# Kernel tuning notes

Measured on AMD Instinct MI355X. Metric: run time of the kernel, lower is better.

The kernel has to match this reference:

```python
import jax, jax.numpy as jnp
import numpy as np

M, NQ, NKV, DX, DT = 8, 1024, 1024, 512, 2
H, HD = 8, 64            # num_heads, head_dim
INNER = H * HD           # 512
KHID = 16                # kernel MLP hidden dim
SCALE = HD ** -0.5


def setup_inputs() -> dict:
    key = jax.random.key(0)
    ks = jax.random.split(key, 16)
    s = lambda fan_in: 1.0 / np.sqrt(fan_in)
    return {
        "xq": jax.random.normal(ks[0], (M, NQ, DX), jnp.float32),
        "xk": jax.random.normal(ks[1], (M, NKV, DX), jnp.float32),
        "xv": jax.random.normal(ks[2], (M, NKV, DX), jnp.float32),
        "tq": jax.random.normal(ks[3], (M, NQ, DT), jnp.float32),
        "tk": jax.random.normal(ks[4], (M, NKV, DT), jnp.float32),
        # attention projections (bias=False for q/k/v, Linear bias for out)
        "w_q": jax.random.normal(ks[5], (DX, INNER), jnp.float32) * s(DX),
        "w_k": jax.random.normal(ks[6], (DX, INNER), jnp.float32) * s(DX),
        "w_v": jax.random.normal(ks[7], (DX, INNER), jnp.float32) * s(DX),
        "w_out": jax.random.normal(ks[8], (INNER, DX), jnp.float32) * s(INNER),
        "b_out": jnp.zeros((DX,), jnp.float32),
        # kernel MLP: dt -> KHID -> H (per-head pairwise bias)
        "kw1": jax.random.normal(ks[9], (DT, KHID), jnp.float32) * s(DT),
        "kb1": jnp.zeros((KHID,), jnp.float32),
        "kw2": jax.random.normal(ks[10], (KHID, H), jnp.float32) * s(KHID),
        "kb2": jnp.zeros((H,), jnp.float32),
    }


def reference(xq, xk, xv, tq, tk, w_q, w_k, w_v, w_out, b_out, kw1, kb1, kw2, kb2):
    # pairwise differences of input locations: [m, nq, nkv, dt]
    diff = tq[:, :, None, :] - tk[:, None, :, :]
    # kernel MLP -> per-head bias, rearranged to [m, h, nq, nkv]
    hmid = jax.nn.relu(diff @ kw1 + kb1)          # [m, nq, nkv, KHID]
    dots = jnp.einsum('mqkc,ch->mhqk', hmid, kw2) + kb2[None, :, None, None]
    # token attention: standard scaled QK scores
    q = (xq @ w_q).reshape(M, NQ, H, HD)          # [m, nq, h, d]
    k = (xk @ w_k).reshape(M, NKV, H, HD)
    token_dots = jnp.einsum('mqhd,mkhd->mhqk', q, k) * SCALE
    dots = dots + token_dots
    attn = jax.nn.softmax(dots, axis=-1)          # softmax over keys
    v = (xv @ w_v).reshape(M, NKV, H, HD)
    out = jnp.einsum('mhqk,mkhd->mqhd', attn, v).reshape(M, NQ, INNER)
    return out @ w_out + b_out                    # [m, nq, dx]
```

## Files before the change

### kernel.cpp

```cpp
#include <hip/hip_runtime.h>


typedef unsigned short u16;
typedef unsigned int   u32;
typedef short bf8 __attribute__((ext_vector_type(8)));
typedef float f4  __attribute__((ext_vector_type(4)));
typedef _Float16 h2 __attribute__((ext_vector_type(2)));

#define Mb 8
#define SCALE 0.125f
#define NTOK 4194304

__device__ __forceinline__ u16 f2bf(float f) {
    union { float f; u32 u; } v; v.f = f;
    u32 r = v.u + 0x7fffu + ((v.u >> 16) & 1u);
    return (u16)(r >> 16);
}
__device__ __forceinline__ u32 pk2(float a, float b) {
    u32 r;
    asm("v_cvt_pk_bf16_f32 %0, %1, %2" : "=v"(r) : "v"(a), "v"(b));
    return r;
}
__device__ __forceinline__ void gl_lds16(const u16* g, u16* l) {
    __builtin_amdgcn_global_load_lds(
        (const __attribute__((address_space(1))) u32*)g,
        (__attribute__((address_space(3))) u32*)l, 16, 0, 0);
}
__device__ __forceinline__ h2 h2_of(u32 x) {
    union { u32 u; h2 h; } c; c.u = x; return c.h;
}
__device__ __forceinline__ u32 u_of(h2 x) {
    union { h2 h; u32 u; } c; c.h = x; return c.u;
}
__device__ __forceinline__ float dot2(h2 a, h2 b, float c) {
#if __has_builtin(__builtin_amdgcn_fdot2)
    return __builtin_amdgcn_fdot2(a, b, c, false);
#else
    return fmaf((float)a[0], (float)b[0], fmaf((float)a[1], (float)b[1], c));
#endif
}

struct PArgs {
    const float* ws[4];
    u16* dstW;
};

__global__ __launch_bounds__(256) void prep(PArgs p) {
    __shared__ u16 tl[64][80];
    const int tid = threadIdx.x;
    const int b = blockIdx.x;
    const int mat = b >> 6, t = b & 63;
    const int kt = t >> 3, nt = t & 7;
    const float* src = p.ws[mat] + (size_t)kt * 64 * 512 + (size_t)nt * 64;
    const int r0 = tid >> 4, c4 = (tid & 15) * 4;
    #pragma unroll
    for (int rr = 0; rr < 4; ++rr) {
        const int row = r0 + rr * 16;
        float4 a = *(const float4*)(src + (size_t)row * 512 + c4);
        tl[c4 + 0][row] = f2bf(a.x);
        tl[c4 + 1][row] = f2bf(a.y);
        tl[c4 + 2][row] = f2bf(a.z);
        tl[c4 + 3][row] = f2bf(a.w);
    }
    __syncthreads();
    u16* dst = p.dstW + (size_t)mat * 262144 + (size_t)nt * 64 * 512 + (size_t)kt * 64;
    #pragma unroll
    for (int i = 0; i < 2; ++i) {
        const int s2 = tid + i * 256;
        const int nrow = s2 >> 3, k8 = (s2 & 7) * 8;
        *(uint4*)(dst + (size_t)nrow * 512 + k8) = *(const uint4*)&tl[nrow][k8];
    }
}

struct GArgs {
    const void*  A[3];
    const u16*   W[3];
    void*        C[3];
    const float* bias;
    int          modeT[3];
    int          outf32;
    int          af32;
};

__global__ __launch_bounds__(256) void gemm_mfma(GArgs g) {
    __shared__ u16 Xs[128][32];
    __shared__ u16 Ws[128][32];

    const int z   = blockIdx.z;
    const int tid = threadIdx.x;
    const int w = tid >> 6, lane = tid & 63, quad = lane >> 4, l16 = lane & 15;
    const int wm = w >> 1, wn = w & 1;
    const int n0 = blockIdx.x * 128, t0 = blockIdx.y * 128;
    const int trans = g.modeT[z];

    f4 acc[4][4];
    #pragma unroll
    for (int i = 0; i < 4; ++i)
        #pragma unroll
        for (int j = 0; j < 4; ++j) acc[i][j] = (f4)0.f;

    const int lrow  = lane >> 2;
    const int kslot = (lane & 3) ^ ((lane >> 3) & 3);
    u16* ldsW0 = &Ws[w * 32][0];
    u16* ldsW1 = &Ws[w * 32 + 16][0];
    const u16* gW0 = g.W[z] + (size_t)(n0 + w * 32 + lrow) * 512 + kslot * 8;
    const u16* gW1 = gW0 + 16 * 512;

    u16* ldsX0 = &Xs[w * 32][0];
    u16* ldsX1 = &Xs[w * 32 + 16][0];
    const u16* gA0 = (const u16*)g.A[z] + (size_t)(t0 + w * 32 + lrow) * 512 + kslot * 8;
    const u16* gA1 = gA0 + 16 * 512;

    const int arow_s = tid >> 1, ah = tid & 1;
    const float* aF = (const float*)g.A[z] + (size_t)(t0 + arow_s) * 512 + ah * 16;
    const int s_sw = (arow_s >> 1) & 3;
    u16* aw0 = &Xs[arow_s][((2 * ah)     ^ s_sw) * 8];
    u16* aw1 = &Xs[arow_s][((2 * ah + 1) ^ s_sw) * 8];

    const int rslot = (quad ^ ((l16 >> 1) & 3)) * 8;

    float4 f0, f1, f2, f3;
    if (g.af32) {
        f0 = *(const float4*)(aF + 0);
        f1 = *(const float4*)(aF + 4);
        f2 = *(const float4*)(aF + 8);
        f3 = *(const float4*)(aF + 12);
    }

    for (int kc = 0; kc < 512; kc += 32) {
        __syncthreads();
        if (g.af32) {
            uint4 v0, v1;
            v0.x = pk2(f0.x, f0.y); v0.y = pk2(f0.z, f0.w);
            v0.z = pk2(f1.x, f1.y); v0.w = pk2(f1.z, f1.w);
            v1.x = pk2(f2.x, f2.y); v1.y = pk2(f2.z, f2.w);
            v1.z = pk2(f3.x, f3.y); v1.w = pk2(f3.z, f3.w);
            *(uint4*)aw0 = v0;
            *(uint4*)aw1 = v1;
        } else {
            gl_lds16(gA0 + kc, ldsX0);
            gl_lds16(gA1 + kc, ldsX1);
        }
        gl_lds16(gW0 + kc, ldsW0);
        gl_lds16(gW1 + kc, ldsW1);
        if (g.af32 && kc + 32 < 512) {
            f0 = *(const float4*)(aF + kc + 32);
            f1 = *(const float4*)(aF + kc + 36);
            f2 = *(const float4*)(aF + kc + 40);
            f3 = *(const float4*)(aF + kc + 44);
        }
        __syncthreads();

        const u16* Abase = trans ? &Xs[0][0] : &Ws[0][0];
        const u16* Bbase = trans ? &Ws[0][0] : &Xs[0][0];
        const int arow = (trans ? wm : wn) * 64;
        const int brow = (trans ? wn : wm) * 64;
        bf8 af[4], bf[4];
        #pragma unroll
        for (int i = 0; i < 4; ++i)
            af[i] = *(const bf8*)(Abase + (arow + i * 16 + l16) * 32 + rslot);
        #pragma unroll
        for (int j = 0; j < 4; ++j)
            bf[j] = *(const bf8*)(Bbase + (brow + j * 16 + l16) * 32 + rslot);
        #pragma unroll
        for (int i = 0; i < 4; ++i)
            #pragma unroll
            for (int j = 0; j < 4; ++j)
                acc[i][j] = __builtin_amdgcn_mfma_f32_16x16x32_bf16(af[i], bf[j], acc[i][j], 0, 0, 0);
    }

    if (g.outf32) {
        float* Co = (float*)g.C[z];
        #pragma unroll
        for (int i = 0; i < 4; ++i) {
            const int nb = n0 + wn * 64 + i * 16 + quad * 4;
            float4 bv = *(const float4*)&g.bias[nb];
            #pragma unroll
            for (int j = 0; j < 4; ++j) {
                const int tok = t0 + wm * 64 + j * 16 + l16;
                float4 st;
                st.x = acc[i][j][0] + bv.x; st.y = acc[i][j][1] + bv.y;
                st.z = acc[i][j][2] + bv.z; st.w = acc[i][j][3] + bv.w;
                *(float4*)&Co[(size_t)tok * 512 + nb] = st;
            }
        }
    } else if (!trans) {
        u16* C = (u16*)g.C[z];
        #pragma unroll
        for (int i = 0; i < 4; ++i) {
            const int nb = n0 + wn * 64 + i * 16 + quad * 4;
            #pragma unroll
            for (int j = 0; j < 4; ++j) {
                const int tok = t0 + wm * 64 + j * 16 + l16;
                uint2 pw;
                pw.x = pk2(acc[i][j][0], acc[i][j][1]);
                pw.y = pk2(acc[i][j][2], acc[i][j][3]);
                *(uint2*)&C[(size_t)tok * 512 + nb] = pw;
            }
        }
    } else {
        u16* Vt = (u16*)g.C[z];
        #pragma unroll
        for (int i = 0; i < 4; ++i) {
            const int tokb = t0 + wm * 64 + i * 16 + quad * 4;
            const int mb = tokb >> 10, tb = tokb & 1023;
            #pragma unroll
            for (int j = 0; j < 4; ++j) {
                const int n = n0 + wn * 64 + j * 16 + l16;
                uint2 pw;
                pw.x = pk2(acc[i][j][0], acc[i][j][1]);
                pw.y = pk2(acc[i][j][2], acc[i][j][3]);
                *(uint2*)&Vt[(size_t)mb * 524288 + (size_t)n * 1024 + tb] = pw;
            }
        }
    }
}

__global__ __launch_bounds__(512) void attn_mfma(
    const u16* __restrict__ Q, const u16* __restrict__ K,
    const u16* __restrict__ Vt,
    const float* __restrict__ tqp, const float* __restrict__ tkp,
    const float* __restrict__ kw1, const float* __restrict__ kb1,
    const float* __restrict__ kw2,
    u16* __restrict__ O)
{
    __shared__ u16 sK[2][8][64][8];
    __shared__ u16 sV[2][8][64][8];
    __shared__ u32 sv2[2][8][68];

    const int tid = threadIdx.x;
    const int w = tid >> 6, lane = tid & 63, quad = lane >> 4, l16 = lane & 15;
    const int b = (blockIdx.z * 8 + blockIdx.y) * 8 + blockIdx.x;
    const int xc = b & 7, j = b >> 3;
    const int hm = xc * 8 + (j & 7);
    const int qt = j >> 3;
    const int h = hm & 7, m = hm >> 3;
    const int q0 = qt * 128;
    const size_t qtok = (size_t)m * 1024 + q0 + w * 16 + l16;

    bf8 qf[2];
    {
        const u16* qp = Q + qtok * 512 + h * 64 + quad * 8;
        qf[0] = *(const bf8*)qp;
        qf[1] = *(const bf8*)(qp + 32);
    }
    h2 u2[8], w2p[8];
    {
        const float t0v = tqp[qtok * 2], t1v = tqp[qtok * 2 + 1];
        #pragma unroll
        for (int cp = 0; cp < 8; ++cp) {
            const int c0 = 2 * cp, c1 = 2 * cp + 1;
            float ua = fmaf(t0v, kw1[c0], fmaf(t1v, kw1[16 + c0], kb1[c0]));
            float ub = fmaf(t0v, kw1[c1], fmaf(t1v, kw1[16 + c1], kb1[c1]));
            u2[cp][0]  = (_Float16)ua;              u2[cp][1]  = (_Float16)ub;
            w2p[cp][0] = (_Float16)kw2[c0 * 8 + h]; w2p[cp][1] = (_Float16)kw2[c1 * 8 + h];
        }
    }
    const float w0a = kw1[2 * w],     w1a = kw1[16 + 2 * w];
    const float w0b = kw1[2 * w + 1], w1b = kw1[16 + 2 * w + 1];

    const u16* gK = K + ((size_t)m * 1024 + lane) * 512 + h * 64 + w * 8;
    const u16* gV = Vt + (size_t)m * 524288 + (size_t)(h * 64 + lane) * 1024 + w * 8;
    const float* gT = tkp + (size_t)m * 2048 + lane * 2;

    float mrun = -1e30f, lrun = 0.f;
    f4 o[4];
    #pragma unroll
    for (int d = 0; d < 4; ++d) o[d] = (f4)0.f;

    auto STAGE = [&](int kt2, int nb) {
        const int k0n = kt2 * 64;
        float2 t = *(const float2*)(gT + k0n * 2);
        h2 pv;
        pv[0] = (_Float16)fmaf(t.x, w0a, t.y * w1a);
        pv[1] = (_Float16)fmaf(t.x, w0b, t.y * w1b);
        sv2[nb][w][lane] = u_of(pv);
        gl_lds16(gK + (size_t)k0n * 512, &sK[nb][w][0][0]);
        gl_lds16(gV + k0n,               &sV[nb][w][0][0]);
    };

    STAGE(0, 0);
    __syncthreads();

    const int la = ((quad & 1) * 2) * 16 + l16;
    const int lb = la + 16;
    const bool hiq = (quad >> 1) != 0;

    int cur = 0;
    for (int kt = 0; kt < 16; ++kt) {
        if (kt < 15) STAGE(kt + 1, cur ^ 1);

        f4 s[4];
        #pragma unroll
        for (int msub = 0; msub < 4; ++msub) {
            bf8 kf0 = *(const bf8*)&sK[cur][quad][msub * 16 + l16][0];
            bf8 kf1 = *(const bf8*)&sK[cur][4 + quad][msub * 16 + l16][0];
            s[msub] = __builtin_amdgcn_mfma_f32_16x16x32_bf16(kf0, qf[0], (f4)0.f, 0, 0, 0);
            s[msub] = __builtin_amdgcn_mfma_f32_16x16x32_bf16(kf1, qf[1], s[msub], 0, 0, 0);
        }
        #pragma unroll
        for (int msub = 0; msub < 4; ++msub) {
            const int kb = msub * 16 + quad * 4;
            f4 b2 = (f4)0.f;
            #pragma unroll
            for (int cp = 0; cp < 8; ++cp) {
                uint4 vv = *(const uint4*)&sv2[cur][cp][kb];
                const h2 uc = u2[cp], wc = w2p[cp];
                const h2 z = (h2)(_Float16)0.f;
                h2 d0 = uc - h2_of(vv.x);
                h2 d1 = uc - h2_of(vv.y);
                h2 d2 = uc - h2_of(vv.z);
                h2 d3 = uc - h2_of(vv.w);
                d0 = __builtin_elementwise_max(d0, z);
                d1 = __builtin_elementwise_max(d1, z);
                d2 = __builtin_elementwise_max(d2, z);
                d3 = __builtin_elementwise_max(d3, z);
                b2[0] = dot2(d0, wc, b2[0]);
                b2[1] = dot2(d1, wc, b2[1]);
                b2[2] = dot2(d2, wc, b2[2]);
                b2[3] = dot2(d3, wc, b2[3]);
            }
            s[msub] = s[msub] * SCALE + b2;
        }
        float mx = -1e30f;
        #pragma unroll
        for (int msub = 0; msub < 4; ++msub) {
            mx = fmaxf(mx, fmaxf(fmaxf(s[msub][0], s[msub][1]),
                                 fmaxf(s[msub][2], s[msub][3])));
        }
        mx = fmaxf(mx, __shfl_xor(mx, 16));
        mx = fmaxf(mx, __shfl_xor(mx, 32));
        const float mnew = fmaxf(mrun, mx);
        float ps = 0.f;
        #pragma unroll
        for (int msub = 0; msub < 4; ++msub) {
            #pragma unroll
            for (int r = 0; r < 4; ++r) {
                float p = __expf(s[msub][r] - mnew);
                s[msub][r] = p;
                ps += p;
            }
        }
        ps += __shfl_xor(ps, 16);
        ps += __shfl_xor(ps, 32);
        if (__all(mx <= mrun)) {
            lrun += ps;
        } else {
            const float alpha = __expf(mrun - mnew);
            lrun = lrun * alpha + ps;
            mrun = mnew;
            #pragma unroll
            for (int d = 0; d < 4; ++d) o[d] = o[d] * alpha;
        }
        uint2 pw0, pw1, pw2, pw3;
        pw0.x = pk2(s[0][0], s[0][1]); pw0.y = pk2(s[0][2], s[0][3]);
        pw1.x = pk2(s[1][0], s[1][1]); pw1.y = pk2(s[1][2], s[1][3]);
        pw2.x = pk2(s[2][0], s[2][1]); pw2.y = pk2(s[2][2], s[2][3]);
        pw3.x = pk2(s[3][0], s[3][1]); pw3.y = pk2(s[3][2], s[3][3]);

        uint4 pf0, pf1;
        {
            u32 a0x = (u32)__shfl((int)pw0.x, la), a0y = (u32)__shfl((int)pw0.y, la);
            u32 b0x = (u32)__shfl((int)pw0.x, lb), b0y = (u32)__shfl((int)pw0.y, lb);
            u32 a1x = (u32)__shfl((int)pw1.x, la), a1y = (u32)__shfl((int)pw1.y, la);
            u32 b1x = (u32)__shfl((int)pw1.x, lb), b1y = (u32)__shfl((int)pw1.y, lb);
            pf0.x = hiq ? a1x : a0x;
            pf0.y = hiq ? a1y : a0y;
            pf0.z = hiq ? b1x : b0x;
            pf0.w = hiq ? b1y : b0y;
            u32 c0x = (u32)__shfl((int)pw2.x, la), c0y = (u32)__shfl((int)pw2.y, la);
            u32 d0x = (u32)__shfl((int)pw2.x, lb), d0y = (u32)__shfl((int)pw2.y, lb);
            u32 c1x = (u32)__shfl((int)pw3.x, la), c1y = (u32)__shfl((int)pw3.y, la);
            u32 d1x = (u32)__shfl((int)pw3.x, lb), d1y = (u32)__shfl((int)pw3.y, lb);
            pf1.x = hiq ? c1x : c0x;
            pf1.y = hiq ? c1y : c0y;
            pf1.z = hiq ? d1x : d0x;
            pf1.w = hiq ? d1y : d0y;
        }
        bf8 pfv0 = *(const bf8*)&pf0;
        bf8 pfv1 = *(const bf8*)&pf1;

        #pragma unroll
        for (int dsub = 0; dsub < 4; ++dsub) {
            bf8 vf0 = *(const bf8*)&sV[cur][quad][dsub * 16 + l16][0];
            bf8 vf1 = *(const bf8*)&sV[cur][4 + quad][dsub * 16 + l16][0];
            o[dsub] = __builtin_amdgcn_mfma_f32_16x16x32_bf16(vf0, pfv0, o[dsub], 0, 0, 0);
            o[dsub] = __builtin_amdgcn_mfma_f32_16x16x32_bf16(vf1, pfv1, o[dsub], 0, 0, 0);
        }

        if (kt < 15) __syncthreads();
        cur ^= 1;
    }

    const float inv = 1.f / lrun;
    #pragma unroll
    for (int dsub = 0; dsub < 4; ++dsub) {
        uint2 pw;
        pw.x = pk2(o[dsub][0] * inv, o[dsub][1] * inv);
        pw.y = pk2(o[dsub][2] * inv, o[dsub][3] * inv);
        *(uint2*)&O[qtok * 512 + h * 64 + dsub * 16 + quad * 4] = pw;
    }
}

extern "C" void kernel_launch(void* const* d_in, const int* in_sizes, int n_in,
                              void* d_out, int out_size, void* d_ws, size_t ws_size,
                              hipStream_t stream) {
    const float* xq    = (const float*)d_in[0];
    const float* xk    = (const float*)d_in[1];
    const float* xv    = (const float*)d_in[2];
    const float* tq    = (const float*)d_in[3];
    const float* tk    = (const float*)d_in[4];
    const float* w_q   = (const float*)d_in[5];
    const float* w_k   = (const float*)d_in[6];
    const float* w_v   = (const float*)d_in[7];
    const float* w_out = (const float*)d_in[8];
    const float* b_out = (const float*)d_in[9];
    const float* kw1   = (const float*)d_in[10];
    const float* kb1   = (const float*)d_in[11];
    const float* kw2   = (const float*)d_in[12];

    u16* Q  = (u16*)d_ws;
    u16* Kp = Q  + NTOK;
    u16* Vt = Kp + NTOK;
    u16* O  = Vt + NTOK;
    u16* Wq = O  + NTOK;
    u16* Wk = Wq + 262144;
    u16* Wv = Wk + 262144;
    u16* Wo = Wv + 262144;

    PArgs p;
    p.ws[0] = w_q; p.ws[1] = w_k; p.ws[2] = w_v; p.ws[3] = w_out;
    p.dstW = Wq;
    prep<<<dim3(256), 256, 0, stream>>>(p);

    GArgs gq;
    gq.A[0] = xq;  gq.A[1] = xk;  gq.A[2] = xv;
    gq.W[0] = Wq;  gq.W[1] = Wk;  gq.W[2] = Wv;
    gq.C[0] = Q;   gq.C[1] = Kp;  gq.C[2] = Vt;
    gq.bias = nullptr;
    gq.modeT[0] = 0; gq.modeT[1] = 0; gq.modeT[2] = 1;
    gq.outf32 = 0; gq.af32 = 1;
    gemm_mfma<<<dim3(4, 64, 3), 256, 0, stream>>>(gq);

    attn_mfma<<<dim3(8, 8, Mb), 512, 0, stream>>>(Q, Kp, Vt, tq, tk,
                                                  kw1, kb1, kw2, O);

    GArgs go;
    go.A[0] = O;   go.A[1] = O;   go.A[2] = O;
    go.W[0] = Wo;  go.W[1] = Wo;  go.W[2] = Wo;
    go.C[0] = d_out; go.C[1] = d_out; go.C[2] = d_out;
    go.bias = b_out;
    go.modeT[0] = 0; go.modeT[1] = 0; go.modeT[2] = 0;
    go.outf32 = 1; go.af32 = 0;
    gemm_mfma<<<dim3(4, 64, 1), 256, 0, stream>>>(go);
}
```

Before: 250.6 us.

## Split attention over key halves and merge partial results in a combine kernel

The attention kernel now splits the key dimension into two halves, doubling the grid from 512 to 1024 blocks. Each block writes unnormalized fp32 partial outputs and its running max/sum, and a new combine kernel merges the two halves with softmax rescaling before writing bf16 O. This is meant to raise occupancy and parallelism on the many-CU GPU. It costs extra fp32 partial-buffer traffic to global memory and one more kernel launch.

```diff
diff --git a/kernel.cpp b/kernel.cpp
--- a/kernel.cpp
+++ b/kernel.cpp
@@ -222,7 +222,7 @@
     const float* __restrict__ tqp, const float* __restrict__ tkp,
     const float* __restrict__ kw1, const float* __restrict__ kb1,
     const float* __restrict__ kw2,
-    u16* __restrict__ O)
+    float* __restrict__ Opart, float2* __restrict__ mlbuf)
 {
     __shared__ u16 sK[2][8][64][8];
     __shared__ u16 sV[2][8][64][8];
@@ -230,12 +230,14 @@
 
     const int tid = threadIdx.x;
     const int w = tid >> 6, lane = tid & 63, quad = lane >> 4, l16 = lane & 15;
-    const int b = (blockIdx.z * 8 + blockIdx.y) * 8 + blockIdx.x;
+    const int b = (blockIdx.z * 8 + blockIdx.y) * 16 + blockIdx.x;
     const int xc = b & 7, j = b >> 3;
     const int hm = xc * 8 + (j & 7);
-    const int qt = j >> 3;
+    const int r2 = j >> 3;
+    const int qt = r2 >> 1, half = r2 & 1;
     const int h = hm & 7, m = hm >> 3;
     const int q0 = qt * 128;
+    const int k0t = half * 8;
     const size_t qtok = (size_t)m * 1024 + q0 + w * 16 + l16;
 
     bf8 qf[2];
@@ -279,7 +281,7 @@
         gl_lds16(gV + k0n,               &sV[nb][w][0][0]);
     };
 
-    STAGE(0, 0);
+    STAGE(k0t, 0);
     __syncthreads();
 
     const int la = ((quad & 1) * 2) * 16 + l16;
@@ -287,8 +289,8 @@
     const bool hiq = (quad >> 1) != 0;
 
     int cur = 0;
-    for (int kt = 0; kt < 16; ++kt) {
-        if (kt < 15) STAGE(kt + 1, cur ^ 1);
+    for (int kt = k0t; kt < k0t + 8; ++kt) {
+        if (kt < k0t + 7) STAGE(kt + 1, cur ^ 1);
 
         f4 s[4];
         #pragma unroll
@@ -388,18 +390,58 @@
             o[dsub] = __builtin_amdgcn_mfma_f32_16x16x32_bf16(vf1, pfv1, o[dsub], 0, 0, 0);
         }
 
-        if (kt < 15) __syncthreads();
+        if (kt < k0t + 7) __syncthreads();
         cur ^= 1;
     }
 
-    const float inv = 1.f / lrun;
+    const int tok = q0 + w * 16 + l16;
+    const size_t pidx = (size_t)(half * 64 + hm) * 1024 + tok;
+    float* Op = Opart + pidx * 64;
     #pragma unroll
     for (int dsub = 0; dsub < 4; ++dsub) {
-        uint2 pw;
-        pw.x = pk2(o[dsub][0] * inv, o[dsub][1] * inv);
-        pw.y = pk2(o[dsub][2] * inv, o[dsub][3] * inv);
-        *(uint2*)&O[qtok * 512 + h * 64 + dsub * 16 + quad * 4] = pw;
-    }
+        float4 st;
+        st.x = o[dsub][0]; st.y = o[dsub][1];
+        st.z = o[dsub][2]; st.w = o[dsub][3];
+        *(float4*)&Op[dsub * 16 + quad * 4] = st;
+    }
+    if (quad == 0) mlbuf[pidx] = make_float2(mrun, lrun);
+}
+
+__global__ __launch_bounds__(256) void combine(
+    const float* __restrict__ Opart, const float2* __restrict__ mlbuf,
+    u16* __restrict__ O)
+{
+    const int idx = blockIdx.x * 256 + threadIdx.x;
+    const int d8 = idx & 7;
+    const int tok = (idx >> 3) & 1023;
+    const int mh = idx >> 13;
+    const size_t p1 = (size_t)mh * 1024 + tok;
+    const size_t p2 = p1 + 64 * 1024;
+    const float2 a = mlbuf[p1];
+    const float2 c = mlbuf[p2];
+    const float M = fmaxf(a.x, c.x);
+    const float w1 = __expf(a.x - M);
+    const float w2 = __expf(c.x - M);
+    const float inv = 1.f / fmaf(a.y, w1, c.y * w2);
+    const float* o1 = Opart + p1 * 64 + d8 * 8;
+    const float* o2 = Opart + p2 * 64 + d8 * 8;
+    float4 x0 = *(const float4*)o1;
+    float4 x1 = *(const float4*)(o1 + 4);
+    float4 y0 = *(const float4*)o2;
+    float4 y1 = *(const float4*)(o2 + 4);
+    float r0 = fmaf(x0.x, w1, y0.x * w2) * inv;
+    float r1 = fmaf(x0.y, w1, y0.y * w2) * inv;
+    float r2 = fmaf(x0.z, w1, y0.z * w2) * inv;
+    float r3 = fmaf(x0.w, w1, y0.w * w2) * inv;
+    float r4 = fmaf(x1.x, w1, y1.x * w2) * inv;
+    float r5 = fmaf(x1.y, w1, y1.y * w2) * inv;
+    float r6 = fmaf(x1.z, w1, y1.z * w2) * inv;
+    float r7 = fmaf(x1.w, w1, y1.w * w2) * inv;
+    uint4 outv;
+    outv.x = pk2(r0, r1); outv.y = pk2(r2, r3);
+    outv.z = pk2(r4, r5); outv.w = pk2(r6, r7);
+    const int m_ = mh >> 3, h_ = mh & 7;
+    *(uint4*)&O[(((size_t)m_ * 1024 + tok) * 8 + h_) * 64 + d8 * 8] = outv;
 }
 
 extern "C" void kernel_launch(void* const* d_in, const int* in_sizes, int n_in,
@@ -427,6 +469,8 @@
     u16* Wk = Wq + 262144;
     u16* Wv = Wk + 262144;
     u16* Wo = Wv + 262144;
+    float*  Opart = (float*)(Wo + 262144);
+    float2* mlbuf = (float2*)(Opart + (size_t)2 * 64 * 1024 * 64);
 
     PArgs p;
     p.ws[0] = w_q; p.ws[1] = w_k; p.ws[2] = w_v; p.ws[3] = w_out;
@@ -442,8 +486,11 @@
     gq.outf32 = 0; gq.af32 = 1;
     gemm_mfma<<<dim3(4, 64, 3), 256, 0, stream>>>(gq);
 
-    attn_mfma<<<dim3(8, 8, Mb), 512, 0, stream>>>(Q, Kp, Vt, tq, tk,
-                                                  kw1, kb1, kw2, O);
+    attn_mfma<<<dim3(16, 8, Mb), 512, 0, stream>>>(Q, Kp, Vt, tq, tk,
+                                                   kw1, kb1, kw2,
+                                                   Opart, mlbuf);
+
+    combine<<<dim3(2048), 256, 0, stream>>>(Opart, mlbuf, O);
 
     GArgs go;
     go.A[0] = O;   go.A[1] = O;   go.A[2] = O;
```

New measurement: 257.8 us. +2.9%, slower.
